# Performance work log

Hardware: AMD Instinct MI355X
Metric: run time of the kernel (lower is better)

The kernel has to match this reference:

```python
import jax, jax.numpy as jnp
import numpy as np

B, S, D = 2, 2048, 1024
H = 16
DH = D // H
FF = 4096
N_NEU = 4096
N_PAT = 64
K = 16          # neuron top-k
KP = 8          # pattern top-k
EPS = 1e-5


def _layer_norm(x, g, b):
    mu = jnp.mean(x, axis=-1, keepdims=True)
    var = jnp.mean((x - mu) ** 2, axis=-1, keepdims=True)
    return (x - mu) * jax.lax.rsqrt(var + EPS) * g + b


def setup_inputs() -> dict:
    key = jax.random.key(0)
    ks = jax.random.split(key, 20)
    sc = 0.02
    lin = lambda k, o, i: jax.random.normal(k, (o, i), jnp.float32) * (1.0 / np.sqrt(i))
    return {
        "x": jax.random.normal(ks[0], (B, S, D), jnp.float32),
        "neurons": jax.random.normal(ks[1], (N_NEU, D), jnp.float32) * sc,
        "wq": lin(ks[2], D, D), "bq": jnp.zeros((D,), jnp.float32),
        "wk": lin(ks[3], D, D), "bk": jnp.zeros((D,), jnp.float32),
        "wv": lin(ks[4], D, D), "bv": jnp.zeros((D,), jnp.float32),
        "wp": lin(ks[5], 2, 2 * D), "bp": jnp.zeros((2,), jnp.float32),
        "pattern_queries": jax.random.normal(ks[6], (N_PAT, D), jnp.float32) * sc,
        "gates": jax.random.normal(ks[7], (N_PAT, FF), jnp.float32) * sc,
        "w_up": lin(ks[8], FF, D), "b_up": jnp.zeros((FF,), jnp.float32),
        "w_down": lin(ks[9], D, FF), "b_down": jnp.zeros((D,), jnp.float32),
        "ln1_g": jnp.ones((D,), jnp.float32), "ln1_b": jnp.zeros((D,), jnp.float32),
        "ln2_g": jnp.ones((D,), jnp.float32), "ln2_b": jnp.zeros((D,), jnp.float32),
    }


def _forward(x, neurons, wq, bq, wk, bk, wv, bv, wp, bp, pattern_queries, gates,
             w_up, b_up, w_down, b_down, ln1_g, ln1_b, ln2_g, ln2_b):
    # ---- NeuronRouter on norm1(x) ----
    normed = _layer_norm(x, ln1_g, ln1_b)
    q = (normed @ wq.T + bq).reshape(B, S, H, DH).transpose(0, 2, 1, 3)
    k = (normed @ wk.T + bk).reshape(B, S, H, DH).transpose(0, 2, 1, 3)
    v = (normed @ wv.T + bv).reshape(B, S, H, DH).transpose(0, 2, 1, 3)
    attn = jax.nn.softmax(jnp.einsum('bhqd,bhkd->bhqk', q, k) / np.sqrt(DH), axis=-1)
    context = jnp.einsum('bhqk,bhkd->bhqd', attn, v).transpose(0, 2, 1, 3).reshape(B, S, D)

    token_scores = normed @ neurons.T                     # [B,S,N]
    context_scores = context @ neurons.T                  # [B,S,N]
    combined = jnp.concatenate([normed, context], axis=-1)
    path_w = jax.nn.softmax(combined @ wp.T + bp, axis=-1)  # [B,S,2]
    scores = path_w[..., 0:1] * token_scores + path_w[..., 1:2] * context_scores

    topk_scores, topk_idx = jax.lax.top_k(scores, K)      # [B,S,K]
    topk_weights = jax.nn.softmax(topk_scores, axis=-1)
    selected = neurons[topk_idx]                          # [B,S,K,D]
    router_out = jnp.einsum('bsk,bskd->bsd', topk_weights, selected)

    x = x + router_out

    # ---- PatternFFN on norm2(x) ----
    normed2 = _layer_norm(x, ln2_g, ln2_b)
    # similarity * neuron weight, summed over K -> pattern scores [B,S,P]
    pattern_scores = jnp.einsum('pd,bskd,bsk->bsp', pattern_queries, selected,
                                topk_weights) / np.sqrt(D)
    pat_scores, pat_idx = jax.lax.top_k(pattern_scores, KP)  # [B,S,KP]
    pat_weights = jax.nn.softmax(pat_scores, axis=-1)
    selected_gates = gates[pat_idx]                       # [B,S,KP,FF]
    ffn_gate = jnp.einsum('bsk,bskf->bsf', pat_weights, selected_gates)

    h = normed2 @ w_up.T + b_up                           # [B,S,FF]
    h = jax.nn.gelu(h * jax.nn.sigmoid(ffn_gate), approximate=False)
    ffn_out = h @ w_down.T + b_down

    return x + ffn_out, topk_idx


def reference(x, neurons, wq, bq, wk, bk, wv, bv, wp, bp, pattern_queries, gates,
              w_up, b_up, w_down, b_down, ln1_g, ln1_b, ln2_g, ln2_b):
    return _forward(x, neurons, wq, bq, wk, bk, wv, bv, wp, bp, pattern_queries,
                    gates, w_up, b_up, w_down, b_down, ln1_g, ln1_b, ln2_g, ln2_b)
```

## Files before the change

kernel.cpp:

```cpp
#include <hip/hip_runtime.h>
#include <math.h>

#define DEV static __device__ __forceinline__

constexpr int S_ = 2048;
constexpr int D_ = 1024;
constexpr int H_ = 16;

typedef __attribute__((ext_vector_type(8))) short bf16x8;
typedef __attribute__((ext_vector_type(4))) float f32x4;
typedef __attribute__((ext_vector_type(8))) short s16x8;

DEV unsigned short f2bf(float x) {
    union { float f; unsigned u; } c; c.f = x;
    const unsigned r = (c.u + 0x7FFFu + ((c.u >> 16) & 1u)) >> 16;
    return (unsigned short)r;
}
DEV float bf2f(unsigned short u) {
    union { unsigned u; float f; } c; c.u = ((unsigned)u) << 16;
    return c.f;
}

DEV float blockReduceSum(float v) {
    #pragma unroll
    for (int m = 1; m < 64; m <<= 1) v += __shfl_xor(v, m, 64);
    __shared__ float wsr[4];
    const int lane = threadIdx.x & 63, wid = threadIdx.x >> 6;
    if (lane == 0) wsr[wid] = v;
    __syncthreads();
    v = wsr[0] + wsr[1] + wsr[2] + wsr[3];
    __syncthreads();
    return v;
}

template<int BF16OUT>
__global__ __launch_bounds__(256)
void ln_k(const float* __restrict__ x, const float* __restrict__ g,
          const float* __restrict__ b, void* __restrict__ o)
{
    const int m = blockIdx.x, tid = threadIdx.x;
    const float* xr = x + (size_t)m * D_;
    const float4 xv = *(const float4*)(xr + tid * 4);
    float s = xv.x + xv.y + xv.z + xv.w;
    s = blockReduceSum(s);
    const float mu = s * (1.0f / 1024.0f);
    const float d0 = xv.x - mu, d1 = xv.y - mu, d2 = xv.z - mu, d3 = xv.w - mu;
    float sq = d0 * d0 + d1 * d1 + d2 * d2 + d3 * d3;
    sq = blockReduceSum(sq);
    const float rstd = rsqrtf(sq * (1.0f / 1024.0f) + 1e-5f);
    const float4 gv = *(const float4*)(g + tid * 4);
    const float4 bv = *(const float4*)(b + tid * 4);
    const float o0 = d0 * rstd * gv.x + bv.x;
    const float o1 = d1 * rstd * gv.y + bv.y;
    const float o2 = d2 * rstd * gv.z + bv.z;
    const float o3 = d3 * rstd * gv.w + bv.w;
    if constexpr (BF16OUT) {
        unsigned short* ob = (unsigned short*)o + (size_t)m * D_ + tid * 4;
        *(ushort4*)ob = make_ushort4(f2bf(o0), f2bf(o1), f2bf(o2), f2bf(o3));
    } else {
        *(float4*)((float*)o + (size_t)m * D_ + tid * 4) = make_float4(o0, o1, o2, o3);
    }
}

template<int MODE>
__global__ __launch_bounds__(256)
void gemm32_k(const float* __restrict__ A, const float* __restrict__ Bw,
              const float* __restrict__ bias, const float* __restrict__ extra,
              float* __restrict__ Cout, int M, int N, int Kd)
{
    __shared__ __align__(16) float As[16][132];
    __shared__ __align__(16) float Bs[16][132];
    const int tid = threadIdx.x;
    const int tx = tid & 15, ty = tid >> 4;
    const int row0 = blockIdx.y * 128, col0 = blockIdx.x * 128;
    const int lr = tid & 127, lk = (tid >> 7) * 8;
    const float* Ap = A + (size_t)(row0 + lr) * Kd + lk;
    const float* Bp = Bw + (size_t)(col0 + lr) * Kd + lk;
    float acc[8][8] = {};

    for (int k0 = 0; k0 < Kd; k0 += 16) {
        const float4 a0 = *(const float4*)(Ap + k0);
        const float4 a1 = *(const float4*)(Ap + k0 + 4);
        const float4 b0 = *(const float4*)(Bp + k0);
        const float4 b1 = *(const float4*)(Bp + k0 + 4);
        __syncthreads();
        As[lk + 0][lr] = a0.x; As[lk + 1][lr] = a0.y; As[lk + 2][lr] = a0.z; As[lk + 3][lr] = a0.w;
        As[lk + 4][lr] = a1.x; As[lk + 5][lr] = a1.y; As[lk + 6][lr] = a1.z; As[lk + 7][lr] = a1.w;
        Bs[lk + 0][lr] = b0.x; Bs[lk + 1][lr] = b0.y; Bs[lk + 2][lr] = b0.z; Bs[lk + 3][lr] = b0.w;
        Bs[lk + 4][lr] = b1.x; Bs[lk + 5][lr] = b1.y; Bs[lk + 6][lr] = b1.z; Bs[lk + 7][lr] = b1.w;
        __syncthreads();
        #pragma unroll
        for (int kk = 0; kk < 16; ++kk) {
            float av[8], bv[8];
            *(float4*)&av[0] = *(const float4*)&As[kk][ty * 8];
            *(float4*)&av[4] = *(const float4*)&As[kk][ty * 8 + 4];
            *(float4*)&bv[0] = *(const float4*)&Bs[kk][tx * 8];
            *(float4*)&bv[4] = *(const float4*)&Bs[kk][tx * 8 + 4];
            #pragma unroll
            for (int r = 0; r < 8; ++r)
                #pragma unroll
                for (int c = 0; c < 8; ++c)
                    acc[r][c] = fmaf(av[r], bv[c], acc[r][c]);
        }
    }

    const int gr0 = row0 + ty * 8, gc0 = col0 + tx * 8;
    if constexpr (MODE == 0) {
        const int hh = gc0 >> 6, dh = gc0 & 63;
        const float4 bias0 = *(const float4*)(bias + gc0);
        const float4 bias1 = *(const float4*)(bias + gc0 + 4);
        #pragma unroll
        for (int r = 0; r < 8; ++r) {
            const int m = gr0 + r;
            const int bb = m >> 11, s = m & (S_ - 1);
            float* dst = Cout + (((size_t)(bb * H_ + hh) * S_ + s) * 64 + dh);
            *(float4*)dst = make_float4(acc[r][0] + bias0.x, acc[r][1] + bias0.y,
                                        acc[r][2] + bias0.z, acc[r][3] + bias0.w);
            *(float4*)(dst + 4) = make_float4(acc[r][4] + bias1.x, acc[r][5] + bias1.y,
                                              acc[r][6] + bias1.z, acc[r][7] + bias1.w);
        }
    } else if constexpr (MODE == 1) {
        #pragma unroll
        for (int r = 0; r < 8; ++r) {
            float* dst = Cout + (size_t)(gr0 + r) * N + gc0;
            *(float4*)dst = make_float4(acc[r][0], acc[r][1], acc[r][2], acc[r][3]);
            *(float4*)(dst + 4) = make_float4(acc[r][4], acc[r][5], acc[r][6], acc[r][7]);
        }
    } else if constexpr (MODE == 2) {
        #pragma unroll
        for (int r = 0; r < 8; ++r) {
            const float rs = extra[2 * (gr0 + r)];
            float* dst = Cout + (size_t)(gr0 + r) * N + gc0;
            *(float4*)dst = make_float4(rs * acc[r][0], rs * acc[r][1],
                                        rs * acc[r][2], rs * acc[r][3]);
            *(float4*)(dst + 4) = make_float4(rs * acc[r][4], rs * acc[r][5],
                                              rs * acc[r][6], rs * acc[r][7]);
        }
    } else {
        #pragma unroll
        for (int r = 0; r < 8; ++r) {
            const float rs = extra[2 * (gr0 + r)];
            float* dst = Cout + (size_t)(gr0 + r) * N + gc0;
            const float4 c0 = *(const float4*)dst;
            const float4 c1 = *(const float4*)(dst + 4);
            *(float4*)dst = make_float4(c0.x + rs * acc[r][0], c0.y + rs * acc[r][1],
                                        c0.z + rs * acc[r][2], c0.w + rs * acc[r][3]);
            *(float4*)(dst + 4) = make_float4(c1.x + rs * acc[r][4], c1.y + rs * acc[r][5],
                                              c1.z + rs * acc[r][6], c1.w + rs * acc[r][7]);
        }
    }
}

__global__ __launch_bounds__(256)
void attn2_k(const float* __restrict__ q, const float* __restrict__ k,
             const float* __restrict__ v, float* __restrict__ ctx)
{
    __shared__ __align__(16) float Qs[64][68];
    __shared__ __align__(16) float Ks[64][68];
    __shared__ __align__(16) float Vs[64][68];
    __shared__ __align__(16) float Ps[64][68];
    const int tid = threadIdx.x;
    const int tx = tid & 15, ty = tid >> 4;
    const int bh = blockIdx.y;
    const int q0 = blockIdx.x * 64;
    const float* qb = q + (size_t)bh * S_ * 64;
    const float* kb = k + (size_t)bh * S_ * 64;
    const float* vb = v + (size_t)bh * S_ * 64;

    {
        const int i = tid & 63, dc = (tid >> 6) * 16;
        const float* src = qb + (size_t)(q0 + i) * 64 + dc;
        const float4 t0 = *(const float4*)(src + 0);
        const float4 t1 = *(const float4*)(src + 4);
        const float4 t2 = *(const float4*)(src + 8);
        const float4 t3 = *(const float4*)(src + 12);
        Qs[dc + 0][i] = t0.x;  Qs[dc + 1][i] = t0.y;  Qs[dc + 2][i] = t0.z;  Qs[dc + 3][i] = t0.w;
        Qs[dc + 4][i] = t1.x;  Qs[dc + 5][i] = t1.y;  Qs[dc + 6][i] = t1.z;  Qs[dc + 7][i] = t1.w;
        Qs[dc + 8][i] = t2.x;  Qs[dc + 9][i] = t2.y;  Qs[dc + 10][i] = t2.z; Qs[dc + 11][i] = t2.w;
        Qs[dc + 12][i] = t3.x; Qs[dc + 13][i] = t3.y; Qs[dc + 14][i] = t3.z; Qs[dc + 15][i] = t3.w;
    }

    float mrow[4] = {-INFINITY, -INFINITY, -INFINITY, -INFINITY};
    float lrow[4] = {0.f, 0.f, 0.f, 0.f};
    float acc[4][4] = {};

    for (int kt = 0; kt < S_; kt += 64) {
        __syncthreads();
        {
            const int j = tid & 63, dc = (tid >> 6) * 16;
            const float* ks = kb + (size_t)(kt + j) * 64 + dc;
            const float* vs = vb + (size_t)(kt + j) * 64 + dc;
            const float4 t0 = *(const float4*)(ks + 0);
            const float4 t1 = *(const float4*)(ks + 4);
            const float4 t2 = *(const float4*)(ks + 8);
            const float4 t3 = *(const float4*)(ks + 12);
            Ks[dc + 0][j] = t0.x;  Ks[dc + 1][j] = t0.y;  Ks[dc + 2][j] = t0.z;  Ks[dc + 3][j] = t0.w;
            Ks[dc + 4][j] = t1.x;  Ks[dc + 5][j] = t1.y;  Ks[dc + 6][j] = t1.z;  Ks[dc + 7][j] = t1.w;
            Ks[dc + 8][j] = t2.x;  Ks[dc + 9][j] = t2.y;  Ks[dc + 10][j] = t2.z; Ks[dc + 11][j] = t2.w;
            Ks[dc + 12][j] = t3.x; Ks[dc + 13][j] = t3.y; Ks[dc + 14][j] = t3.z; Ks[dc + 15][j] = t3.w;
            *(float4*)&Vs[j][dc + 0] = *(const float4*)(vs + 0);
            *(float4*)&Vs[j][dc + 4] = *(const float4*)(vs + 4);
            *(float4*)&Vs[j][dc + 8] = *(const float4*)(vs + 8);
            *(float4*)&Vs[j][dc + 12] = *(const float4*)(vs + 12);
        }
        __syncthreads();

        float s[4][4] = {};
        #pragma unroll 8
        for (int d = 0; d < 64; ++d) {
            const float4 q4 = *(const float4*)&Qs[d][ty * 4];
            const float4 k4 = *(const float4*)&Ks[d][tx * 4];
            s[0][0] = fmaf(q4.x, k4.x, s[0][0]); s[0][1] = fmaf(q4.x, k4.y, s[0][1]);
            s[0][2] = fmaf(q4.x, k4.z, s[0][2]); s[0][3] = fmaf(q4.x, k4.w, s[0][3]);
            s[1][0] = fmaf(q4.y, k4.x, s[1][0]); s[1][1] = fmaf(q4.y, k4.y, s[1][1]);
            s[1][2] = fmaf(q4.y, k4.z, s[1][2]); s[1][3] = fmaf(q4.y, k4.w, s[1][3]);
            s[2][0] = fmaf(q4.z, k4.x, s[2][0]); s[2][1] = fmaf(q4.z, k4.y, s[2][1]);
            s[2][2] = fmaf(q4.z, k4.z, s[2][2]); s[2][3] = fmaf(q4.z, k4.w, s[2][3]);
            s[3][0] = fmaf(q4.w, k4.x, s[3][0]); s[3][1] = fmaf(q4.w, k4.y, s[3][1]);
            s[3][2] = fmaf(q4.w, k4.z, s[3][2]); s[3][3] = fmaf(q4.w, k4.w, s[3][3]);
        }

        #pragma unroll
        for (int r = 0; r < 4; ++r) {
            float s0 = s[r][0] * 0.125f, s1 = s[r][1] * 0.125f;
            float s2 = s[r][2] * 0.125f, s3 = s[r][3] * 0.125f;
            float rm = fmaxf(fmaxf(s0, s1), fmaxf(s2, s3));
            #pragma unroll
            for (int sh = 1; sh < 16; sh <<= 1) rm = fmaxf(rm, __shfl_xor(rm, sh, 64));
            const float mn = fmaxf(mrow[r], rm);
            const float p0 = expf(s0 - mn), p1 = expf(s1 - mn);
            const float p2 = expf(s2 - mn), p3 = expf(s3 - mn);
            float rs = p0 + p1 + p2 + p3;
            #pragma unroll
            for (int sh = 1; sh < 16; sh <<= 1) rs += __shfl_xor(rs, sh, 64);
            const float esc = expf(mrow[r] - mn);
            lrow[r] = lrow[r] * esc + rs;
            mrow[r] = mn;
            acc[r][0] *= esc; acc[r][1] *= esc; acc[r][2] *= esc; acc[r][3] *= esc;
            *(float4*)&Ps[ty * 4 + r][tx * 4] = make_float4(p0, p1, p2, p3);
        }
        __syncthreads();

        #pragma unroll 4
        for (int jb = 0; jb < 16; ++jb) {
            const float4 v0 = *(const float4*)&Vs[jb * 4 + 0][tx * 4];
            const float4 v1 = *(const float4*)&Vs[jb * 4 + 1][tx * 4];
            const float4 v2 = *(const float4*)&Vs[jb * 4 + 2][tx * 4];
            const float4 v3 = *(const float4*)&Vs[jb * 4 + 3][tx * 4];
            #pragma unroll
            for (int r = 0; r < 4; ++r) {
                const float4 p4 = *(const float4*)&Ps[ty * 4 + r][jb * 4];
                acc[r][0] = fmaf(p4.x, v0.x, acc[r][0]); acc[r][1] = fmaf(p4.x, v0.y, acc[r][1]);
                acc[r][2] = fmaf(p4.x, v0.z, acc[r][2]); acc[r][3] = fmaf(p4.x, v0.w, acc[r][3]);
                acc[r][0] = fmaf(p4.y, v1.x, acc[r][0]); acc[r][1] = fmaf(p4.y, v1.y, acc[r][1]);
                acc[r][2] = fmaf(p4.y, v1.z, acc[r][2]); acc[r][3] = fmaf(p4.y, v1.w, acc[r][3]);
                acc[r][0] = fmaf(p4.z, v2.x, acc[r][0]); acc[r][1] = fmaf(p4.z, v2.y, acc[r][1]);
                acc[r][2] = fmaf(p4.z, v2.z, acc[r][2]); acc[r][3] = fmaf(p4.z, v2.w, acc[r][3]);
                acc[r][0] = fmaf(p4.w, v3.x, acc[r][0]); acc[r][1] = fmaf(p4.w, v3.y, acc[r][1]);
                acc[r][2] = fmaf(p4.w, v3.z, acc[r][2]); acc[r][3] = fmaf(p4.w, v3.w, acc[r][3]);
            }
        }
    }

    const int bb = bh >> 4, hh = bh & 15;
    #pragma unroll
    for (int r = 0; r < 4; ++r) {
        const float inv = 1.0f / lrow[r];
        *(float4*)(ctx + (size_t)(bb * S_ + q0 + ty * 4 + r) * D_ + hh * 64 + tx * 4) =
            make_float4(acc[r][0] * inv, acc[r][1] * inv, acc[r][2] * inv, acc[r][3] * inv);
    }
}

__global__ __launch_bounds__(256)
void pathw_k(const float* __restrict__ normed, const float* __restrict__ ctx,
             const float* __restrict__ wp, const float* __restrict__ bp,
             float* __restrict__ pw)
{
    const int m = blockIdx.x, tid = threadIdx.x;
    const float4 n4 = *(const float4*)(normed + (size_t)m * D_ + tid * 4);
    const float4 c4 = *(const float4*)(ctx + (size_t)m * D_ + tid * 4);
    const float4 w0n = *(const float4*)(wp + tid * 4);
    const float4 w0c = *(const float4*)(wp + 1024 + tid * 4);
    const float4 w1n = *(const float4*)(wp + 2048 + tid * 4);
    const float4 w1c = *(const float4*)(wp + 3072 + tid * 4);
    float p0 = n4.x * w0n.x + n4.y * w0n.y + n4.z * w0n.z + n4.w * w0n.w
             + c4.x * w0c.x + c4.y * w0c.y + c4.z * w0c.z + c4.w * w0c.w;
    float p1 = n4.x * w1n.x + n4.y * w1n.y + n4.z * w1n.z + n4.w * w1n.w
             + c4.x * w1c.x + c4.y * w1c.y + c4.z * w1c.z + c4.w * w1c.w;
    p0 = blockReduceSum(p0);
    p1 = blockReduceSum(p1);
    if (tid == 0) {
        const float l0 = p0 + bp[0], l1 = p1 + bp[1];
        const float mx = fmaxf(l0, l1);
        const float e0 = expf(l0 - mx), e1 = expf(l1 - mx);
        const float inv = 1.0f / (e0 + e1);
        pw[2 * m] = e0 * inv;
        pw[2 * m + 1] = e1 * inv;
    }
}

__global__ __launch_bounds__(256)
void topk_router_k(const float* __restrict__ scores, const float* __restrict__ neurons,
                   const float* __restrict__ x, float* __restrict__ idx_out,
                   float* __restrict__ x1, float* __restrict__ router)
{
    __shared__ __align__(16) float sc[4096];
    __shared__ unsigned long long wred[4];
    __shared__ int ki_s[16];
    __shared__ float kv_s[16];
    __shared__ float kw_s[16];
    const int m = blockIdx.x, tid = threadIdx.x;
    const float* srow = scores + (size_t)m * 4096;
    for (int i = tid; i < 1024; i += 256)
        *(float4*)&sc[i * 4] = *(const float4*)(srow + i * 4);
    __syncthreads();

    for (int t = 0; t < 16; ++t) {
        unsigned long long best = 0ull;
        for (int i = tid; i < 4096; i += 256) {
            unsigned u = __float_as_uint(sc[i]);
            u = (u & 0x80000000u) ? ~u : (u | 0x80000000u);
            const unsigned long long key =
                ((unsigned long long)u << 32) | (unsigned long long)(0xFFFFFFFFu - (unsigned)i);
            if (key > best) best = key;
        }
        #pragma unroll
        for (int sh = 1; sh < 64; sh <<= 1) {
            const unsigned long long o = __shfl_xor(best, sh, 64);
            if (o > best) best = o;
        }
        if ((tid & 63) == 0) wred[tid >> 6] = best;
        __syncthreads();
        if (tid == 0) {
            unsigned long long bb = wred[0];
            if (wred[1] > bb) bb = wred[1];
            if (wred[2] > bb) bb = wred[2];
            if (wred[3] > bb) bb = wred[3];
            const int idx = (int)(0xFFFFFFFFu - (unsigned)(bb & 0xFFFFFFFFull));
            ki_s[t] = idx;
            kv_s[t] = sc[idx];
            sc[idx] = -INFINITY;
        }
        __syncthreads();
    }

    if (tid == 0) {
        const float mx = kv_s[0];
        float es[16], sum = 0.f;
        #pragma unroll
        for (int t = 0; t < 16; ++t) { es[t] = expf(kv_s[t] - mx); sum += es[t]; }
        const float inv = 1.0f / sum;
        #pragma unroll
        for (int t = 0; t < 16; ++t) kw_s[t] = es[t] * inv;
    }
    __syncthreads();

    if (tid < 16) idx_out[(size_t)m * 16 + tid] = (float)ki_s[tid];

    float4 r = make_float4(0.f, 0.f, 0.f, 0.f);
    #pragma unroll
    for (int t = 0; t < 16; ++t) {
        const float w = kw_s[t];
        const float4 nv = *(const float4*)(neurons + (size_t)ki_s[t] * D_ + tid * 4);
        r.x = fmaf(w, nv.x, r.x); r.y = fmaf(w, nv.y, r.y);
        r.z = fmaf(w, nv.z, r.z); r.w = fmaf(w, nv.w, r.w);
    }
    const float4 xv = *(const float4*)(x + (size_t)m * D_ + tid * 4);
    *(float4*)(router + (size_t)m * D_ + tid * 4) = r;
    *(float4*)(x1 + (size_t)m * D_ + tid * 4) =
        make_float4(xv.x + r.x, xv.y + r.y, xv.z + r.z, xv.w + r.w);
}

__global__ __launch_bounds__(256)
void pattern_k(const float* __restrict__ router, const float* __restrict__ pq,
               const float* __restrict__ gates, unsigned short* __restrict__ gate_out)
{
    __shared__ __align__(16) float rr[1024];
    __shared__ float ps[64];
    __shared__ int pidx[8];
    __shared__ float pwt[8];
    const int m = blockIdx.x, tid = threadIdx.x;
    *(float4*)&rr[tid * 4] = *(const float4*)(router + (size_t)m * D_ + tid * 4);
    __syncthreads();

    const int p = tid >> 2, part = tid & 3;
    const float* pqr = pq + (size_t)p * D_ + part * 256;
    float sum = 0.f;
    for (int d = 0; d < 256; d += 4) {
        const float4 a = *(const float4*)(pqr + d);
        const float4 b = *(const float4*)&rr[part * 256 + d];
        sum += a.x * b.x + a.y * b.y + a.z * b.z + a.w * b.w;
    }
    sum += __shfl_xor(sum, 1, 64);
    sum += __shfl_xor(sum, 2, 64);
    if (part == 0) ps[p] = sum * (1.0f / 32.0f);
    __syncthreads();

    if (tid == 0) {
        float kv[8];
        for (int t = 0; t < 8; ++t) {
            float bv = -INFINITY; int bi = 0;
            for (int i = 0; i < 64; ++i) {
                const float vv = ps[i];
                if (vv > bv) { bv = vv; bi = i; }
            }
            kv[t] = bv; pidx[t] = bi; ps[bi] = -INFINITY;
        }
        const float mx = kv[0];
        float ee[8], tot = 0.f;
        for (int t = 0; t < 8; ++t) { ee[t] = expf(kv[t] - mx); tot += ee[t]; }
        for (int t = 0; t < 8; ++t) pwt[t] = ee[t] / tot;
    }
    __syncthreads();

    for (int f = tid * 4; f < 4096; f += 1024) {
        float4 g = make_float4(0.f, 0.f, 0.f, 0.f);
        #pragma unroll
        for (int t = 0; t < 8; ++t) {
            const float w = pwt[t];
            const float4 gv = *(const float4*)(gates + (size_t)pidx[t] * 4096 + f);
            g.x = fmaf(w, gv.x, g.x); g.y = fmaf(w, gv.y, g.y);
            g.z = fmaf(w, gv.z, g.z); g.w = fmaf(w, gv.w, g.w);
        }
        *(ushort4*)(gate_out + (size_t)m * 4096 + f) =
            make_ushort4(f2bf(g.x), f2bf(g.y), f2bf(g.z), f2bf(g.w));
    }
}

__global__ __launch_bounds__(256)
void castbf_k(const float* __restrict__ in, unsigned short* __restrict__ out, int n)
{
    const int i = (blockIdx.x * 256 + threadIdx.x) * 8;
    if (i >= n) return;
    const float4 a = *(const float4*)(in + i);
    const float4 b = *(const float4*)(in + i + 4);
    *(ushort4*)(out + i) = make_ushort4(f2bf(a.x), f2bf(a.y), f2bf(a.z), f2bf(a.w));
    *(ushort4*)(out + i + 4) = make_ushort4(f2bf(b.x), f2bf(b.y), f2bf(b.z), f2bf(b.w));
}

template<int EPI>
__global__ __launch_bounds__(256)
void gemmbf_k(const unsigned short* __restrict__ A, const unsigned short* __restrict__ Bw,
              const float* __restrict__ bias, const unsigned short* __restrict__ gate,
              const float* resid, void* Cout, int M, int N, int Kd)
{
    __shared__ __align__(16) unsigned short Al[128 * 32];
    __shared__ __align__(16) unsigned short Bl[128 * 32];
    const int tid = threadIdx.x;
    const int lane = tid & 63;
    const int w = tid >> 6, wr = w >> 1, wc = w & 1;
    const int row0 = blockIdx.y * 128, col0 = blockIdx.x * 128;

    const int o0 = tid * 16, o1 = o0 + 4096;
    const int r0 = o0 >> 6, k0e = (o0 & 63) >> 1;
    const int r1 = o1 >> 6, k1e = (o1 & 63) >> 1;
    const unsigned short* Ap0 = A + (size_t)(row0 + r0) * Kd + k0e;
    const unsigned short* Ap1 = A + (size_t)(row0 + r1) * Kd + k1e;
    const unsigned short* Bp0 = Bw + (size_t)(col0 + r0) * Kd + k0e;
    const unsigned short* Bp1 = Bw + (size_t)(col0 + r1) * Kd + k1e;

    f32x4 acc[4][4];
    #pragma unroll
    for (int m = 0; m < 4; ++m)
        #pragma unroll
        for (int n = 0; n < 4; ++n)
            #pragma unroll
            for (int e = 0; e < 4; ++e) acc[m][n][e] = 0.f;

    s16x8 ra0 = *(const s16x8*)Ap0;
    s16x8 ra1 = *(const s16x8*)Ap1;
    s16x8 rb0 = *(const s16x8*)Bp0;
    s16x8 rb1 = *(const s16x8*)Bp1;

    const int fr = lane & 15, kg = (lane >> 4) * 8;
    const unsigned short* aBase = Al + ((wr * 64 + fr) * 32 + kg);
    const unsigned short* bBase = Bl + ((wc * 64 + fr) * 32 + kg);

    for (int k0 = 0; k0 < Kd; k0 += 32) {
        __syncthreads();
        *(s16x8*)(Al + (o0 >> 1)) = ra0;
        *(s16x8*)(Al + (o1 >> 1)) = ra1;
        *(s16x8*)(Bl + (o0 >> 1)) = rb0;
        *(s16x8*)(Bl + (o1 >> 1)) = rb1;
        __syncthreads();
        if (k0 + 32 < Kd) {
            ra0 = *(const s16x8*)(Ap0 + k0 + 32);
            ra1 = *(const s16x8*)(Ap1 + k0 + 32);
            rb0 = *(const s16x8*)(Bp0 + k0 + 32);
            rb1 = *(const s16x8*)(Bp1 + k0 + 32);
        }
        bf16x8 aF[4], bF[4];
        #pragma unroll
        for (int m = 0; m < 4; ++m) aF[m] = *(const bf16x8*)(aBase + m * 16 * 32);
        #pragma unroll
        for (int n = 0; n < 4; ++n) bF[n] = *(const bf16x8*)(bBase + n * 16 * 32);
        #pragma unroll
        for (int m = 0; m < 4; ++m)
            #pragma unroll
            for (int n = 0; n < 4; ++n)
                acc[m][n] = __builtin_amdgcn_mfma_f32_16x16x32_bf16(aF[m], bF[n], acc[m][n], 0, 0, 0);
    }

    const int rbase = (lane >> 4) * 4;
    #pragma unroll
    for (int m = 0; m < 4; ++m) {
        #pragma unroll
        for (int n = 0; n < 4; ++n) {
            const int gcol = col0 + wc * 64 + n * 16 + (lane & 15);
            const int growb = row0 + wr * 64 + m * 16 + rbase;
            const float bc = bias[gcol];
            #pragma unroll
            for (int r = 0; r < 4; ++r) {
                const int grow = growb + r;
                const float vv = acc[m][n][r];
                if constexpr (EPI == 0) {
                    const float z = vv + bc;
                    const float gt = bf2f(gate[(size_t)grow * N + gcol]);
                    const float zz = z / (1.f + expf(-gt));
                    const float o = 0.5f * zz * (1.f + erff(zz * 0.70710678118654752440f));
                    ((unsigned short*)Cout)[(size_t)grow * N + gcol] = f2bf(o);
                } else {
                    ((float*)Cout)[(size_t)grow * N + gcol] =
                        vv + bc + resid[(size_t)grow * N + gcol];
                }
            }
        }
    }
}

extern "C" void kernel_launch(void* const* d_in, const int* in_sizes, int n_in,
                              void* d_out, int out_size, void* d_ws, size_t ws_size,
                              hipStream_t stream)
{
    const float* x      = (const float*)d_in[0];
    const float* neurons= (const float*)d_in[1];
    const float* wq = (const float*)d_in[2];  const float* bq = (const float*)d_in[3];
    const float* wk = (const float*)d_in[4];  const float* bk = (const float*)d_in[5];
    const float* wv = (const float*)d_in[6];  const float* bv = (const float*)d_in[7];
    const float* wp = (const float*)d_in[8];  const float* bp = (const float*)d_in[9];
    const float* pq = (const float*)d_in[10];
    const float* gates = (const float*)d_in[11];
    const float* w_up = (const float*)d_in[12];  const float* b_up = (const float*)d_in[13];
    const float* w_dn = (const float*)d_in[14];  const float* b_dn = (const float*)d_in[15];
    const float* ln1g = (const float*)d_in[16];  const float* ln1b = (const float*)d_in[17];
    const float* ln2g = (const float*)d_in[18];  const float* ln2b = (const float*)d_in[19];

    float* out0    = (float*)d_out;
    float* idx_out = out0 + (size_t)4096 * 1024;

    float* ws      = (float*)d_ws;
    float* scores  = ws;
    float* normed  = ws + 16777216;
    float* qb      = ws + 20971520;
    float* kb      = ws + 25165824;
    float* vb      = ws + 29360128;
    float* ctx     = ws + 33554432;
    float* router  = ws + 37748736;
    float* pw      = ws + 41943040;

    unsigned short* gate_bf   = (unsigned short*)qb;
    unsigned short* h_bf      = (unsigned short*)scores;
    unsigned short* normed2bf = (unsigned short*)(scores + 8388608);
    unsigned short* wup_bf    = (unsigned short*)router;
    unsigned short* wdn_bf    = wup_bf + 4194304;
    float* x1 = out0;

    const dim3 blk(256);

    ln_k<0><<<4096, blk, 0, stream>>>(x, ln1g, ln1b, normed);
    gemm32_k<0><<<dim3(8, 32), blk, 0, stream>>>(normed, wq, bq, nullptr, qb, 4096, 1024, 1024);
    gemm32_k<0><<<dim3(8, 32), blk, 0, stream>>>(normed, wk, bk, nullptr, kb, 4096, 1024, 1024);
    gemm32_k<0><<<dim3(8, 32), blk, 0, stream>>>(normed, wv, bv, nullptr, vb, 4096, 1024, 1024);
    attn2_k<<<dim3(32, 32), blk, 0, stream>>>(qb, kb, vb, ctx);
    pathw_k<<<4096, blk, 0, stream>>>(normed, ctx, wp, bp, pw);
    gemm32_k<2><<<dim3(32, 32), blk, 0, stream>>>(normed, neurons, nullptr, pw, scores, 4096, 4096, 1024);
    gemm32_k<3><<<dim3(32, 32), blk, 0, stream>>>(ctx, neurons, nullptr, pw + 1, scores, 4096, 4096, 1024);
    topk_router_k<<<4096, blk, 0, stream>>>(scores, neurons, x, idx_out, x1, router);
    ln_k<1><<<4096, blk, 0, stream>>>(x1, ln2g, ln2b, normed2bf);
    pattern_k<<<4096, blk, 0, stream>>>(router, pq, gates, gate_bf);
    castbf_k<<<2048, blk, 0, stream>>>(w_up, wup_bf, 4194304);
    castbf_k<<<2048, blk, 0, stream>>>(w_dn, wdn_bf, 4194304);
    gemmbf_k<0><<<dim3(32, 32), blk, 0, stream>>>(normed2bf, wup_bf, b_up, gate_bf, nullptr, h_bf, 4096, 4096, 1024);
    gemmbf_k<1><<<dim3(8, 32), blk, 0, stream>>>(h_bf, wdn_bf, b_dn, nullptr, x1, out0, 4096, 1024, 4096);
}
```

Measured before the change: 2.227 ms.

## Prefetch next tiles into registers in fp32 GEMM and attention, pad bf16 LDS

The fp32 GEMM now works on a K-tile of 32 and loads the next tile into registers while the current one is computed. The attention kernel prefetches the next K/V block into registers the same way, so global load latency overlaps the math. The bf16 MFMA GEMM pads its LDS rows from 32 to 40 elements to reduce bank conflicts on fragment reads. The cost is more registers and LDS per block, which may lower occupancy.

```diff
diff --git a/kernel.cpp b/kernel.cpp
--- a/kernel.cpp
+++ b/kernel.cpp
@@ -68,29 +68,46 @@
               const float* __restrict__ bias, const float* __restrict__ extra,
               float* __restrict__ Cout, int M, int N, int Kd)
 {
-    __shared__ __align__(16) float As[16][132];
-    __shared__ __align__(16) float Bs[16][132];
+    __shared__ __align__(16) float As[32][132];
+    __shared__ __align__(16) float Bs[32][132];
     const int tid = threadIdx.x;
     const int tx = tid & 15, ty = tid >> 4;
     const int row0 = blockIdx.y * 128, col0 = blockIdx.x * 128;
-    const int lr = tid & 127, lk = (tid >> 7) * 8;
+    const int lr = tid & 127, lk = (tid >> 7) * 16;
     const float* Ap = A + (size_t)(row0 + lr) * Kd + lk;
     const float* Bp = Bw + (size_t)(col0 + lr) * Kd + lk;
     float acc[8][8] = {};
 
-    for (int k0 = 0; k0 < Kd; k0 += 16) {
-        const float4 a0 = *(const float4*)(Ap + k0);
-        const float4 a1 = *(const float4*)(Ap + k0 + 4);
-        const float4 b0 = *(const float4*)(Bp + k0);
-        const float4 b1 = *(const float4*)(Bp + k0 + 4);
-        __syncthreads();
-        As[lk + 0][lr] = a0.x; As[lk + 1][lr] = a0.y; As[lk + 2][lr] = a0.z; As[lk + 3][lr] = a0.w;
-        As[lk + 4][lr] = a1.x; As[lk + 5][lr] = a1.y; As[lk + 6][lr] = a1.z; As[lk + 7][lr] = a1.w;
-        Bs[lk + 0][lr] = b0.x; Bs[lk + 1][lr] = b0.y; Bs[lk + 2][lr] = b0.z; Bs[lk + 3][lr] = b0.w;
-        Bs[lk + 4][lr] = b1.x; Bs[lk + 5][lr] = b1.y; Bs[lk + 6][lr] = b1.z; Bs[lk + 7][lr] = b1.w;
-        __syncthreads();
-        #pragma unroll
-        for (int kk = 0; kk < 16; ++kk) {
+    float4 ar[4], br[4];
+    #pragma unroll
+    for (int jj = 0; jj < 4; ++jj) {
+        ar[jj] = *(const float4*)(Ap + jj * 4);
+        br[jj] = *(const float4*)(Bp + jj * 4);
+    }
+
+    for (int k0 = 0; k0 < Kd; k0 += 32) {
+        __syncthreads();
+        #pragma unroll
+        for (int jj = 0; jj < 4; ++jj) {
+            As[lk + jj * 4 + 0][lr] = ar[jj].x;
+            As[lk + jj * 4 + 1][lr] = ar[jj].y;
+            As[lk + jj * 4 + 2][lr] = ar[jj].z;
+            As[lk + jj * 4 + 3][lr] = ar[jj].w;
+            Bs[lk + jj * 4 + 0][lr] = br[jj].x;
+            Bs[lk + jj * 4 + 1][lr] = br[jj].y;
+            Bs[lk + jj * 4 + 2][lr] = br[jj].z;
+            Bs[lk + jj * 4 + 3][lr] = br[jj].w;
+        }
+        __syncthreads();
+        if (k0 + 32 < Kd) {
+            #pragma unroll
+            for (int jj = 0; jj < 4; ++jj) {
+                ar[jj] = *(const float4*)(Ap + k0 + 32 + jj * 4);
+                br[jj] = *(const float4*)(Bp + k0 + 32 + jj * 4);
+            }
+        }
+        #pragma unroll
+        for (int kk = 0; kk < 32; ++kk) {
             float av[8], bv[8];
             *(float4*)&av[0] = *(const float4*)&As[kk][ty * 8];
             *(float4*)&av[4] = *(const float4*)&As[kk][ty * 8 + 4];
@@ -118,13 +135,6 @@
                                         acc[r][2] + bias0.z, acc[r][3] + bias0.w);
             *(float4*)(dst + 4) = make_float4(acc[r][4] + bias1.x, acc[r][5] + bias1.y,
                                               acc[r][6] + bias1.z, acc[r][7] + bias1.w);
-        }
-    } else if constexpr (MODE == 1) {
-        #pragma unroll
-        for (int r = 0; r < 8; ++r) {
-            float* dst = Cout + (size_t)(gr0 + r) * N + gc0;
-            *(float4*)dst = make_float4(acc[r][0], acc[r][1], acc[r][2], acc[r][3]);
-            *(float4*)(dst + 4) = make_float4(acc[r][4], acc[r][5], acc[r][6], acc[r][7]);
         }
     } else if constexpr (MODE == 2) {
         #pragma unroll
@@ -152,7 +162,7 @@
 }
 
 __global__ __launch_bounds__(256)
-void attn2_k(const float* __restrict__ q, const float* __restrict__ k,
+void attn3_k(const float* __restrict__ q, const float* __restrict__ k,
              const float* __restrict__ v, float* __restrict__ ctx)
 {
     __shared__ __align__(16) float Qs[64][68];
@@ -167,17 +177,28 @@
     const float* kb = k + (size_t)bh * S_ * 64;
     const float* vb = v + (size_t)bh * S_ * 64;
 
+    const int j = tid & 63, dc = (tid >> 6) * 16;
+
     {
-        const int i = tid & 63, dc = (tid >> 6) * 16;
-        const float* src = qb + (size_t)(q0 + i) * 64 + dc;
+        const float* src = qb + (size_t)(q0 + j) * 64 + dc;
         const float4 t0 = *(const float4*)(src + 0);
         const float4 t1 = *(const float4*)(src + 4);
         const float4 t2 = *(const float4*)(src + 8);
         const float4 t3 = *(const float4*)(src + 12);
-        Qs[dc + 0][i] = t0.x;  Qs[dc + 1][i] = t0.y;  Qs[dc + 2][i] = t0.z;  Qs[dc + 3][i] = t0.w;
-        Qs[dc + 4][i] = t1.x;  Qs[dc + 5][i] = t1.y;  Qs[dc + 6][i] = t1.z;  Qs[dc + 7][i] = t1.w;
-        Qs[dc + 8][i] = t2.x;  Qs[dc + 9][i] = t2.y;  Qs[dc + 10][i] = t2.z; Qs[dc + 11][i] = t2.w;
-        Qs[dc + 12][i] = t3.x; Qs[dc + 13][i] = t3.y; Qs[dc + 14][i] = t3.z; Qs[dc + 15][i] = t3.w;
+        Qs[dc + 0][j] = t0.x;  Qs[dc + 1][j] = t0.y;  Qs[dc + 2][j] = t0.z;  Qs[dc + 3][j] = t0.w;
+        Qs[dc + 4][j] = t1.x;  Qs[dc + 5][j] = t1.y;  Qs[dc + 6][j] = t1.z;  Qs[dc + 7][j] = t1.w;
+        Qs[dc + 8][j] = t2.x;  Qs[dc + 9][j] = t2.y;  Qs[dc + 10][j] = t2.z; Qs[dc + 11][j] = t2.w;
+        Qs[dc + 12][j] = t3.x; Qs[dc + 13][j] = t3.y; Qs[dc + 14][j] = t3.z; Qs[dc + 15][j] = t3.w;
+    }
+
+    float4 kr0, kr1, kr2, kr3, vr0, vr1, vr2, vr3;
+    {
+        const float* ks = kb + (size_t)j * 64 + dc;
+        const float* vs = vb + (size_t)j * 64 + dc;
+        kr0 = *(const float4*)(ks + 0);  kr1 = *(const float4*)(ks + 4);
+        kr2 = *(const float4*)(ks + 8);  kr3 = *(const float4*)(ks + 12);
+        vr0 = *(const float4*)(vs + 0);  vr1 = *(const float4*)(vs + 4);
+        vr2 = *(const float4*)(vs + 8);  vr3 = *(const float4*)(vs + 12);
     }
 
     float mrow[4] = {-INFINITY, -INFINITY, -INFINITY, -INFINITY};
@@ -186,24 +207,24 @@
 
     for (int kt = 0; kt < S_; kt += 64) {
         __syncthreads();
-        {
-            const int j = tid & 63, dc = (tid >> 6) * 16;
-            const float* ks = kb + (size_t)(kt + j) * 64 + dc;
-            const float* vs = vb + (size_t)(kt + j) * 64 + dc;
-            const float4 t0 = *(const float4*)(ks + 0);
-            const float4 t1 = *(const float4*)(ks + 4);
-            const float4 t2 = *(const float4*)(ks + 8);
-            const float4 t3 = *(const float4*)(ks + 12);
-            Ks[dc + 0][j] = t0.x;  Ks[dc + 1][j] = t0.y;  Ks[dc + 2][j] = t0.z;  Ks[dc + 3][j] = t0.w;
-            Ks[dc + 4][j] = t1.x;  Ks[dc + 5][j] = t1.y;  Ks[dc + 6][j] = t1.z;  Ks[dc + 7][j] = t1.w;
-            Ks[dc + 8][j] = t2.x;  Ks[dc + 9][j] = t2.y;  Ks[dc + 10][j] = t2.z; Ks[dc + 11][j] = t2.w;
-            Ks[dc + 12][j] = t3.x; Ks[dc + 13][j] = t3.y; Ks[dc + 14][j] = t3.z; Ks[dc + 15][j] = t3.w;
-            *(float4*)&Vs[j][dc + 0] = *(const float4*)(vs + 0);
-            *(float4*)&Vs[j][dc + 4] = *(const float4*)(vs + 4);
-            *(float4*)&Vs[j][dc + 8] = *(const float4*)(vs + 8);
-            *(float4*)&Vs[j][dc + 12] = *(const float4*)(vs + 12);
-        }
-        __syncthreads();
+        Ks[dc + 0][j] = kr0.x;  Ks[dc + 1][j] = kr0.y;  Ks[dc + 2][j] = kr0.z;  Ks[dc + 3][j] = kr0.w;
+        Ks[dc + 4][j] = kr1.x;  Ks[dc + 5][j] = kr1.y;  Ks[dc + 6][j] = kr1.z;  Ks[dc + 7][j] = kr1.w;
+        Ks[dc + 8][j] = kr2.x;  Ks[dc + 9][j] = kr2.y;  Ks[dc + 10][j] = kr2.z; Ks[dc + 11][j] = kr2.w;
+        Ks[dc + 12][j] = kr3.x; Ks[dc + 13][j] = kr3.y; Ks[dc + 14][j] = kr3.z; Ks[dc + 15][j] = kr3.w;
+        *(float4*)&Vs[j][dc + 0]  = vr0;
+        *(float4*)&Vs[j][dc + 4]  = vr1;
+        *(float4*)&Vs[j][dc + 8]  = vr2;
+        *(float4*)&Vs[j][dc + 12] = vr3;
+        __syncthreads();
+
+        if (kt + 64 < S_) {
+            const float* ks = kb + (size_t)(kt + 64 + j) * 64 + dc;
+            const float* vs = vb + (size_t)(kt + 64 + j) * 64 + dc;
+            kr0 = *(const float4*)(ks + 0);  kr1 = *(const float4*)(ks + 4);
+            kr2 = *(const float4*)(ks + 8);  kr3 = *(const float4*)(ks + 12);
+            vr0 = *(const float4*)(vs + 0);  vr1 = *(const float4*)(vs + 4);
+            vr2 = *(const float4*)(vs + 8);  vr3 = *(const float4*)(vs + 12);
+        }
 
         float s[4][4] = {};
         #pragma unroll 8
@@ -444,8 +465,9 @@
               const float* __restrict__ bias, const unsigned short* __restrict__ gate,
               const float* resid, void* Cout, int M, int N, int Kd)
 {
-    __shared__ __align__(16) unsigned short Al[128 * 32];
-    __shared__ __align__(16) unsigned short Bl[128 * 32];
+    constexpr int LSH = 40;
+    __shared__ __align__(16) unsigned short Al[128 * LSH];
+    __shared__ __align__(16) unsigned short Bl[128 * LSH];
     const int tid = threadIdx.x;
     const int lane = tid & 63;
     const int w = tid >> 6, wr = w >> 1, wc = w & 1;
@@ -454,6 +476,7 @@
     const int o0 = tid * 16, o1 = o0 + 4096;
     const int r0 = o0 >> 6, k0e = (o0 & 63) >> 1;
     const int r1 = o1 >> 6, k1e = (o1 & 63) >> 1;
+    const int l0 = r0 * LSH + k0e, l1 = r1 * LSH + k1e;
     const unsigned short* Ap0 = A + (size_t)(row0 + r0) * Kd + k0e;
     const unsigned short* Ap1 = A + (size_t)(row0 + r1) * Kd + k1e;
     const unsigned short* Bp0 = Bw + (size_t)(col0 + r0) * Kd + k0e;
@@ -473,15 +496,15 @@
     s16x8 rb1 = *(const s16x8*)Bp1;
 
     const int fr = lane & 15, kg = (lane >> 4) * 8;
-    const unsigned short* aBase = Al + ((wr * 64 + fr) * 32 + kg);
-    const unsigned short* bBase = Bl + ((wc * 64 + fr) * 32 + kg);
+    const unsigned short* aBase = Al + ((wr * 64 + fr) * LSH + kg);
+    const unsigned short* bBase = Bl + ((wc * 64 + fr) * LSH + kg);
 
     for (int k0 = 0; k0 < Kd; k0 += 32) {
         __syncthreads();
-        *(s16x8*)(Al + (o0 >> 1)) = ra0;
-        *(s16x8*)(Al + (o1 >> 1)) = ra1;
-        *(s16x8*)(Bl + (o0 >> 1)) = rb0;
-        *(s16x8*)(Bl + (o1 >> 1)) = rb1;
+        *(s16x8*)(Al + l0) = ra0;
+        *(s16x8*)(Al + l1) = ra1;
+        *(s16x8*)(Bl + l0) = rb0;
+        *(s16x8*)(Bl + l1) = rb1;
         __syncthreads();
         if (k0 + 32 < Kd) {
             ra0 = *(const s16x8*)(Ap0 + k0 + 32);
@@ -491,9 +514,9 @@
         }
         bf16x8 aF[4], bF[4];
         #pragma unroll
-        for (int m = 0; m < 4; ++m) aF[m] = *(const bf16x8*)(aBase + m * 16 * 32);
-        #pragma unroll
-        for (int n = 0; n < 4; ++n) bF[n] = *(const bf16x8*)(bBase + n * 16 * 32);
+        for (int m = 0; m < 4; ++m) aF[m] = *(const bf16x8*)(aBase + m * 16 * LSH);
+        #pragma unroll
+        for (int n = 0; n < 4; ++n) bF[n] = *(const bf16x8*)(bBase + n * 16 * LSH);
         #pragma unroll
         for (int m = 0; m < 4; ++m)
             #pragma unroll
@@ -571,7 +594,7 @@
     gemm32_k<0><<<dim3(8, 32), blk, 0, stream>>>(normed, wq, bq, nullptr, qb, 4096, 1024, 1024);
     gemm32_k<0><<<dim3(8, 32), blk, 0, stream>>>(normed, wk, bk, nullptr, kb, 4096, 1024, 1024);
     gemm32_k<0><<<dim3(8, 32), blk, 0, stream>>>(normed, wv, bv, nullptr, vb, 4096, 1024, 1024);
-    attn2_k<<<dim3(32, 32), blk, 0, stream>>>(qb, kb, vb, ctx);
+    attn3_k<<<dim3(32, 32), blk, 0, stream>>>(qb, kb, vb, ctx);
     pathw_k<<<4096, blk, 0, stream>>>(normed, ctx, wp, bp, pw);
     gemm32_k<2><<<dim3(32, 32), blk, 0, stream>>>(normed, neurons, nullptr, pw, scores, 4096, 4096, 1024);
     gemm32_k<3><<<dim3(32, 32), blk, 0, stream>>>(ctx, neurons, nullptr, pw + 1, scores, 4096, 4096, 1024);
```

After: 2.110 ms. -5.3%, faster.
